# Kernel tuning notes

Measured on AMD Instinct MI355X. Metric: run time of the kernel, lower is better.

Reference implementation:

```python
import jax, jax.numpy as jnp
import numpy as np

NHEAD = 8  # from init_kwargs
EPS = 1e-5  # nn.LayerNorm default


def _ln(x, w, b):
    mu = jnp.mean(x, axis=-1, keepdims=True)
    var = jnp.mean(jnp.square(x - mu), axis=-1, keepdims=True)
    return (x - mu) * jax.lax.rsqrt(var + EPS) * w + b


def setup_inputs() -> dict:
    key = jax.random.key(0)
    L, D, FF, B, S = 4, 256, 512, 2, 4096
    ks = jax.random.split(key, 14)
    s = 0.02
    inp = {
        "seq": jax.random.normal(ks[0], (B, S, D), jnp.float32),
        "Wqkv": jax.random.normal(ks[1], (L, 3 * D, D), jnp.float32) * s,
        "bqkv": jnp.zeros((L, 3 * D), jnp.float32),
        "Wo": jax.random.normal(ks[2], (L, D, D), jnp.float32) * s,
        "bo": jnp.zeros((L, D), jnp.float32),
        "ln1_w": jnp.ones((L, D), jnp.float32),
        "ln1_b": jnp.zeros((L, D), jnp.float32),
        "ln2_w": jnp.ones((L, D), jnp.float32),
        "ln2_b": jnp.zeros((L, D), jnp.float32),
        "W1": jax.random.normal(ks[3], (L, FF, D), jnp.float32) * s,
        "b1": jnp.zeros((L, FF), jnp.float32),
        "W2": jax.random.normal(ks[4], (L, D, FF), jnp.float32) * s,
        "b2": jnp.zeros((L, D), jnp.float32),
        "n_ctx": 2048,
    }
    return inp


def _forward(seq, Wqkv, bqkv, Wo, bo, ln1_w, ln1_b, ln2_w, ln2_b, W1, b1, W2, b2, n_ctx):
    B, S, D = seq.shape
    H = NHEAD
    hd = D // H
    scale = 1.0 / np.sqrt(hd).astype(np.float32)
    x = seq
    L = Wqkv.shape[0]
    for l in range(L):
        # pre-norm self-attention block (norm_first=True)
        h = _ln(x, ln1_w[l], ln1_b[l])
        qkv = h @ Wqkv[l].T + bqkv[l]            # [B,S,3D]
        q, k, v = jnp.split(qkv, 3, axis=-1)
        q = q.reshape(B, S, H, hd)
        # Mask structure: every token (context AND query) may only attend to
        # context keys [:n_ctx] -> keys/values restricted up-front, no dense
        # [S,S] score matrix and no explicit mask needed.
        kc = k[:, :n_ctx].reshape(B, n_ctx, H, hd)
        vc = v[:, :n_ctx].reshape(B, n_ctx, H, hd)
        scores = jnp.einsum('bqhd,bkhd->bhqk', q, kc) * scale  # [B,H,S,n_ctx]
        att = jax.nn.softmax(scores, axis=-1)
        o = jnp.einsum('bhqk,bkhd->bqhd', att, vc).reshape(B, S, D)
        x = x + o @ Wo[l].T + bo[l]
        # pre-norm feed-forward block, exact (erf) GELU as in PyTorch 'gelu'
        h2 = _ln(x, ln2_w[l], ln2_b[l])
        x = x + jax.nn.gelu(h2 @ W1[l].T + b1[l], approximate=False) @ W2[l].T + b2[l]
    return x


def reference(seq, Wqkv, bqkv, Wo, bo, ln1_w, ln1_b, ln2_w, ln2_b, W1, b1, W2, b2, n_ctx):
    return _forward(seq, Wqkv, bqkv, Wo, bo, ln1_w, ln1_b, ln2_w, ln2_b, W1, b1, W2, b2, n_ctx)
```

## Files before the change

### kernel.cpp

```cpp
#include <hip/hip_runtime.h>
#include <hip/hip_bf16.h>

#define BB 2
#define SS 4096
#define DD 256
#define FFD 512
#define NLAYER 4
#define NHEAD 8
#define HD 32
#define QKVD 768
#define NROWS 8192
#define NCTX 2048

typedef unsigned short u16;
typedef unsigned int   u32;
typedef __attribute__((ext_vector_type(8))) short short8;
typedef __attribute__((ext_vector_type(4))) short sv4;
typedef __attribute__((ext_vector_type(4))) float f32x4;

#if __has_builtin(__builtin_amdgcn_exp2f)
#define EXP2(x) __builtin_amdgcn_exp2f(x)
#else
#define EXP2(x) exp2f(x)
#endif

__device__ __forceinline__ float bf2f(u32 u) { return __uint_as_float(u << 16); }
__device__ __forceinline__ u16 f2bu(float f) {
    union { __hip_bfloat16 h; u16 u; } cv; cv.h = __float2bfloat16(f); return cv.u;
}
__device__ __forceinline__ float gelu_f(float v) {
    return 0.5f * v * (1.0f + erff(v * 0.70710678118654752f));
}

__global__ __launch_bounds__(256) void init_kernel(
        const float* __restrict__ s0, const float* __restrict__ s1,
        const float* __restrict__ s2, const float* __restrict__ s3,
        u16* __restrict__ d0, u16* __restrict__ d1,
        u16* __restrict__ d2, u16* __restrict__ d3,
        const float* __restrict__ seq, float* __restrict__ x,
        const float* __restrict__ lw, const float* __restrict__ lb,
        u16* __restrict__ hln) {
    int blk = blockIdx.x;
    if (blk < 2048) {
        const float* s; u16* d; int base;
        if (blk < 768)       { s = s0; d = d0; base = blk; }
        else if (blk < 1024) { s = s1; d = d1; base = blk - 768; }
        else if (blk < 1536) { s = s2; d = d2; base = blk - 1024; }
        else                 { s = s3; d = d3; base = blk - 1536; }
        int i = (base * 256 + threadIdx.x) * 4;
        float4 v = *reinterpret_cast<const float4*>(s + i);
        uint2 o;
        o.x = (u32)f2bu(v.x) | ((u32)f2bu(v.y) << 16);
        o.y = (u32)f2bu(v.z) | ((u32)f2bu(v.w) << 16);
        *reinterpret_cast<uint2*>(d + i) = o;
    } else {
        int row = (blk - 2048) * 4 + (threadIdx.x >> 6);
        int lane = threadIdx.x & 63;
        int c = lane * 4;
        float4 v = *reinterpret_cast<const float4*>(seq + (size_t)row * DD + c);
        *reinterpret_cast<float4*>(x + (size_t)row * DD + c) = v;
        float s  = v.x + v.y + v.z + v.w;
        float sq = v.x*v.x + v.y*v.y + v.z*v.z + v.w*v.w;
        #pragma unroll
        for (int off = 32; off >= 1; off >>= 1) {
            s  += __shfl_xor(s, off);
            sq += __shfl_xor(sq, off);
        }
        float mu   = s * (1.0f / DD);
        float var  = sq * (1.0f / DD) - mu * mu;
        float rstd = rsqrtf(var + 1e-5f);
        float4 wv = *reinterpret_cast<const float4*>(lw + c);
        float4 bv = *reinterpret_cast<const float4*>(lb + c);
        float o0 = (v.x - mu) * rstd * wv.x + bv.x;
        float o1 = (v.y - mu) * rstd * wv.y + bv.y;
        float o2 = (v.z - mu) * rstd * wv.z + bv.z;
        float o3 = (v.w - mu) * rstd * wv.w + bv.w;
        uint2 o;
        o.x = (u32)f2bu(o0) | ((u32)f2bu(o1) << 16);
        o.y = (u32)f2bu(o2) | ((u32)f2bu(o3) << 16);
        *reinterpret_cast<uint2*>(hln + (size_t)row * DD + c) = o;
    }
}

__global__ void ln_kernel(const float* __restrict__ x, const float* __restrict__ w,
                          const float* __restrict__ b, u16* __restrict__ out) {
    int row = blockIdx.x * 4 + (threadIdx.x >> 6);
    int lane = threadIdx.x & 63;
    int c = lane * 4;
    float4 v = *reinterpret_cast<const float4*>(x + (size_t)row * DD + c);
    float s  = v.x + v.y + v.z + v.w;
    float sq = v.x*v.x + v.y*v.y + v.z*v.z + v.w*v.w;
    #pragma unroll
    for (int off = 32; off >= 1; off >>= 1) {
        s  += __shfl_xor(s, off);
        sq += __shfl_xor(sq, off);
    }
    float mu   = s * (1.0f / DD);
    float var  = sq * (1.0f / DD) - mu * mu;
    float rstd = rsqrtf(var + 1e-5f);
    float4 wv = *reinterpret_cast<const float4*>(w + c);
    float4 bv = *reinterpret_cast<const float4*>(b + c);
    float o0 = (v.x - mu) * rstd * wv.x + bv.x;
    float o1 = (v.y - mu) * rstd * wv.y + bv.y;
    float o2 = (v.z - mu) * rstd * wv.z + bv.z;
    float o3 = (v.w - mu) * rstd * wv.w + bv.w;
    uint2 o;
    o.x = (u32)f2bu(o0) | ((u32)f2bu(o1) << 16);
    o.y = (u32)f2bu(o2) | ((u32)f2bu(o3) << 16);
    *reinterpret_cast<uint2*>(out + (size_t)row * DD + c) = o;
}

template<int TM, int ACT, int RES, int WV>
__global__ __launch_bounds__(256) void mfma_gemm(
        const u16* __restrict__ A, const u16* __restrict__ W, const float* __restrict__ bias,
        float* __restrict__ outf, u16* __restrict__ outb, u16* __restrict__ vtg,
        int N, int K) {
    constexpr int MI = TM / 32;
    __shared__ __align__(16) u16 As[TM][136];
    __shared__ __align__(16) u16 Ws[64][136];
    int tid = threadIdx.x;
    int wave = tid >> 6, lane = tid & 63, la = lane & 15, quad = lane >> 4;
    int wm = (wave & 1) * (TM / 2), wn = (wave >> 1) * 32;
    int m0 = blockIdx.y * TM, n0 = blockIdx.x * 64;
    f32x4 acc[MI][2];
    #pragma unroll
    for (int mi = 0; mi < MI; mi++)
        #pragma unroll
        for (int ni = 0; ni < 2; ni++)
            acc[mi][ni] = (f32x4){0.f, 0.f, 0.f, 0.f};

    int ar = tid >> 4, ac = (tid & 15) * 8;
    for (int k0 = 0; k0 < K; k0 += 128) {
        #pragma unroll
        for (int p = 0; p < TM / 16; p++)
            *reinterpret_cast<uint4*>(&As[ar + p*16][ac]) =
                *reinterpret_cast<const uint4*>(&A[(size_t)(m0 + ar + p*16) * K + k0 + ac]);
        #pragma unroll
        for (int p = 0; p < 4; p++)
            *reinterpret_cast<uint4*>(&Ws[ar + p*16][ac]) =
                *reinterpret_cast<const uint4*>(&W[(size_t)(n0 + ar + p*16) * K + k0 + ac]);
        __syncthreads();
        #pragma unroll
        for (int kh = 0; kh < 4; kh++) {
            short8 af[MI], bf[2];
            #pragma unroll
            for (int mi = 0; mi < MI; mi++)
                af[mi] = *reinterpret_cast<const short8*>(&As[wm + mi*16 + la][kh*32 + quad*8]);
            #pragma unroll
            for (int ni = 0; ni < 2; ni++)
                bf[ni] = *reinterpret_cast<const short8*>(&Ws[wn + ni*16 + la][kh*32 + quad*8]);
            #pragma unroll
            for (int mi = 0; mi < MI; mi++)
                #pragma unroll
                for (int ni = 0; ni < 2; ni++)
                    acc[mi][ni] = __builtin_amdgcn_mfma_f32_16x16x32_bf16(af[mi], bf[ni], acc[mi][ni], 0, 0, 0);
        }
        __syncthreads();
    }

    #pragma unroll
    for (int mi = 0; mi < MI; mi++) {
        #pragma unroll
        for (int ni = 0; ni < 2; ni++) {
            int n = n0 + wn + ni*16 + la;
            float bv = bias[n];
            #pragma unroll
            for (int r = 0; r < 4; r++) {
                int m = m0 + wm + mi*16 + quad*4 + r;
                float v = acc[mi][ni][r] + bv;
                if (ACT) v = gelu_f(v);
                if (RES) outf[(size_t)m * N + n] += v;
                else     outb[(size_t)m * N + n] = f2bu(v);
            }
        }
    }

    if (WV) {
        if ((n0 >= 2*DD) && ((m0 & (SS-1)) < NCTX)) {
            int b = m0 >> 12;
            int kb = ((m0 + wm) & (SS-1)) + quad*8;
            #pragma unroll
            for (int mi = 0; mi < MI; mi++) {
                int chunk = kb + (mi >> 1)*32 + (mi & 1)*4;
                #pragma unroll
                for (int ni = 0; ni < 2; ni++) {
                    int n = n0 + wn + ni*16 + la;
                    int vc = n - 2*DD;
                    float bv = bias[n];
                    u16* dst = &vtg[((size_t)((b << 3) + (vc >> 5)) * 32 + (vc & 31)) * NCTX + chunk];
                    uint2 w;
                    w.x = (u32)f2bu(acc[mi][ni][0] + bv) | ((u32)f2bu(acc[mi][ni][1] + bv) << 16);
                    w.y = (u32)f2bu(acc[mi][ni][2] + bv) | ((u32)f2bu(acc[mi][ni][3] + bv) << 16);
                    *reinterpret_cast<uint2*>(dst) = w;
                }
            }
        }
    }
}

#define SCL2 0.2550437f
#define SH2  11.5415603f
__global__ __launch_bounds__(512, 4) void mfma_attn(const u16* __restrict__ qkv,
                                                    const u16* __restrict__ vtg,
                                                    u16* __restrict__ out) {
    __shared__ __align__(16) u16 smem[9728];
    u16 (*Ks)[64][40] = reinterpret_cast<u16(*)[64][40]>(smem);
    u16 (*Vt)[32][72] = reinterpret_cast<u16(*)[32][72]>(smem + 5120);

    int tid = threadIdx.x;
    int wv = tid >> 6, lane = tid & 63, la = lane & 15, quad = lane >> 4;
    int qw = wv & 3, ksp = wv >> 2;
    int bh = blockIdx.y, qidx = blockIdx.x;
    int b = bh >> 3, hh = bh & 7;
    size_t tokbase = (size_t)b * SS;
    int qb = qidx * 128 + qw * 32;

    short8 qf[2];
    #pragma unroll
    for (int qt = 0; qt < 2; qt++) {
        uint4 u = *reinterpret_cast<const uint4*>(
            &qkv[(tokbase + qb + qt*16 + la) * QKVD + hh*32 + quad*8]);
        union { short8 v; u16 e[8]; } qa;
        u32 w[4] = {u.x, u.y, u.z, u.w};
        #pragma unroll
        for (int i = 0; i < 4; i++) {
            qa.e[2*i]   = f2bu(bf2f(w[i] & 0xffffu) * SCL2);
            qa.e[2*i+1] = f2bu(bf2f(w[i] >> 16) * SCL2);
        }
        qf[qt] = qa.v;
    }

    f32x4 o[2][2];
    #pragma unroll
    for (int i = 0; i < 2; i++)
        #pragma unroll
        for (int j = 0; j < 2; j++) o[i][j] = (f32x4){0.f, 0.f, 0.f, 0.f};
    f32x4 l_acc[2];
    l_acc[0] = (f32x4){0.f, 0.f, 0.f, 0.f};
    l_acc[1] = (f32x4){0.f, 0.f, 0.f, 0.f};
    const f32x4 cinit = (f32x4){-SH2, -SH2, -SH2, -SH2};
    short8 onesf;
    { union { short8 v; u16 e[8]; } t;
      #pragma unroll
      for (int i = 0; i < 8; i++) t.e[i] = 0x3F80;
      onesf = t.v; }

    int sr = tid >> 2, sk = (tid & 3) * 8;
    int hs = sr >> 6, krow = sr & 63;
    int vr = tid >> 4, vc = (tid & 15) * 8;
    int vh = vc >> 6, vcol = vc & 63;
    const u16* kgp = &qkv[(tokbase + hs*1024 + krow) * QKVD + DD + hh*32 + sk];
    const u16* vgp = &vtg[((size_t)bh*32 + vr) * NCTX + vh*1024 + vcol];
    uint4 kreg = *reinterpret_cast<const uint4*>(kgp);
    uint4 vreg = *reinterpret_cast<const uint4*>(vgp);

    for (int step = 0; step < 16; step++) {
        *reinterpret_cast<uint4*>(&Ks[hs][krow][sk]) = kreg;
        *reinterpret_cast<uint4*>(&Vt[vh][vr][vcol]) = vreg;
        __syncthreads();
        if (step < 15) {
            kreg = *reinterpret_cast<const uint4*>(kgp + (size_t)(step+1)*64*QKVD);
            vreg = *reinterpret_cast<const uint4*>(vgp + (step+1)*64);
        }

        #pragma unroll
        for (int c = 0; c < 2; c++) {
            short8 kf0 = *reinterpret_cast<const short8*>(&Ks[ksp][c*32 + la][quad*8]);
            short8 kf1 = *reinterpret_cast<const short8*>(&Ks[ksp][c*32 + 16 + la][quad*8]);
            f32x4 s00 = __builtin_amdgcn_mfma_f32_16x16x32_bf16(kf0, qf[0], cinit, 0, 0, 0);
            f32x4 s10 = __builtin_amdgcn_mfma_f32_16x16x32_bf16(kf1, qf[0], cinit, 0, 0, 0);
            f32x4 s01 = __builtin_amdgcn_mfma_f32_16x16x32_bf16(kf0, qf[1], cinit, 0, 0, 0);
            f32x4 s11 = __builtin_amdgcn_mfma_f32_16x16x32_bf16(kf1, qf[1], cinit, 0, 0, 0);

            union { uint4 u; short8 v; } pf0, pf1;
            {
                u32 a0 = __float_as_uint(EXP2(s00[0])), a1 = __float_as_uint(EXP2(s00[1]));
                u32 a2 = __float_as_uint(EXP2(s00[2])), a3 = __float_as_uint(EXP2(s00[3]));
                u32 b0 = __float_as_uint(EXP2(s10[0])), b1 = __float_as_uint(EXP2(s10[1]));
                u32 b2 = __float_as_uint(EXP2(s10[2])), b3 = __float_as_uint(EXP2(s10[3]));
                pf0.u.x = __builtin_amdgcn_perm(a1, a0, 0x07060302u);
                pf0.u.y = __builtin_amdgcn_perm(a3, a2, 0x07060302u);
                pf0.u.z = __builtin_amdgcn_perm(b1, b0, 0x07060302u);
                pf0.u.w = __builtin_amdgcn_perm(b3, b2, 0x07060302u);
            }
            {
                u32 a0 = __float_as_uint(EXP2(s01[0])), a1 = __float_as_uint(EXP2(s01[1]));
                u32 a2 = __float_as_uint(EXP2(s01[2])), a3 = __float_as_uint(EXP2(s01[3]));
                u32 b0 = __float_as_uint(EXP2(s11[0])), b1 = __float_as_uint(EXP2(s11[1]));
                u32 b2 = __float_as_uint(EXP2(s11[2])), b3 = __float_as_uint(EXP2(s11[3]));
                pf1.u.x = __builtin_amdgcn_perm(a1, a0, 0x07060302u);
                pf1.u.y = __builtin_amdgcn_perm(a3, a2, 0x07060302u);
                pf1.u.z = __builtin_amdgcn_perm(b1, b0, 0x07060302u);
                pf1.u.w = __builtin_amdgcn_perm(b3, b2, 0x07060302u);
            }

            l_acc[0] = __builtin_amdgcn_mfma_f32_16x16x32_bf16(onesf, pf0.v, l_acc[0], 0, 0, 0);
            l_acc[1] = __builtin_amdgcn_mfma_f32_16x16x32_bf16(onesf, pf1.v, l_acc[1], 0, 0, 0);

            short8 vf0 = *reinterpret_cast<const short8*>(&Vt[ksp][la][c*32 + quad*8]);
            short8 vf1 = *reinterpret_cast<const short8*>(&Vt[ksp][16 + la][c*32 + quad*8]);
            o[0][0] = __builtin_amdgcn_mfma_f32_16x16x32_bf16(vf0, pf0.v, o[0][0], 0, 0, 0);
            o[0][1] = __builtin_amdgcn_mfma_f32_16x16x32_bf16(vf0, pf1.v, o[0][1], 0, 0, 0);
            o[1][0] = __builtin_amdgcn_mfma_f32_16x16x32_bf16(vf1, pf0.v, o[1][0], 0, 0, 0);
            o[1][1] = __builtin_amdgcn_mfma_f32_16x16x32_bf16(vf1, pf1.v, o[1][1], 0, 0, 0);
        }
        __syncthreads();
    }

    float* obuf = reinterpret_cast<float*>(smem);
    if (wv >= 4) {
        int idx = (qw * 64 + lane) * 18;
        #pragma unroll
        for (int mio = 0; mio < 2; mio++)
            #pragma unroll
            for (int qt = 0; qt < 2; qt++)
                #pragma unroll
                for (int r = 0; r < 4; r++)
                    obuf[idx + mio*8 + qt*4 + r] = o[mio][qt][r];
        obuf[idx + 16] = l_acc[0][0];
        obuf[idx + 17] = l_acc[1][0];
    }
    __syncthreads();
    if (wv < 4) {
        int idx = (qw * 64 + lane) * 18;
        #pragma unroll
        for (int mio = 0; mio < 2; mio++)
            #pragma unroll
            for (int qt = 0; qt < 2; qt++)
                #pragma unroll
                for (int r = 0; r < 4; r++)
                    o[mio][qt][r] += obuf[idx + mio*8 + qt*4 + r];
        float liq[2];
        liq[0] = 1.0f / (l_acc[0][0] + obuf[idx + 16]);
        liq[1] = 1.0f / (l_acc[1][0] + obuf[idx + 17]);
        #pragma unroll
        for (int qt = 0; qt < 2; qt++) {
            float li = liq[qt];
            size_t token = tokbase + qb + qt*16 + la;
            #pragma unroll
            for (int mio = 0; mio < 2; mio++) {
                uint2 w;
                w.x = (u32)f2bu(o[mio][qt][0] * li) | ((u32)f2bu(o[mio][qt][1] * li) << 16);
                w.y = (u32)f2bu(o[mio][qt][2] * li) | ((u32)f2bu(o[mio][qt][3] * li) << 16);
                *reinterpret_cast<uint2*>(&out[token * DD + hh*32 + mio*16 + quad*4]) = w;
            }
        }
    }
}

extern "C" void kernel_launch(void* const* d_in, const int* in_sizes, int n_in,
                              void* d_out, int out_size, void* d_ws, size_t ws_size,
                              hipStream_t stream) {
    const float* seq   = (const float*)d_in[0];
    const float* Wqkv  = (const float*)d_in[1];
    const float* bqkv  = (const float*)d_in[2];
    const float* Wo    = (const float*)d_in[3];
    const float* bo    = (const float*)d_in[4];
    const float* ln1w  = (const float*)d_in[5];
    const float* ln1b  = (const float*)d_in[6];
    const float* ln2w  = (const float*)d_in[7];
    const float* ln2b  = (const float*)d_in[8];
    const float* W1    = (const float*)d_in[9];
    const float* b1    = (const float*)d_in[10];
    const float* W2    = (const float*)d_in[11];
    const float* b2    = (const float*)d_in[12];

    float* x    = (float*)d_out;
    char* wsb   = (char*)d_ws;
    u16*  qkv   = (u16*)wsb;
    u16*  ff    = qkv;
    u16*  h     = (u16*)(wsb + 12582912);
    u16*  hln   = (u16*)(wsb + 16777216);
    u16*  wbf   = (u16*)(wsb + 20971520);
    u16*  vtg   = (u16*)(wsb + 25165824);
    u16* wqkv_b = wbf;
    u16* wo_b   = wbf + 786432;
    u16* w1_b   = wbf + 1048576;
    u16* w2_b   = wbf + 1572864;

    init_kernel<<<4096, 256, 0, stream>>>(Wqkv, Wo, W1, W2, wqkv_b, wo_b, w1_b, w2_b,
                                          seq, x, ln1w, ln1b, hln);

    for (int l = 0; l < NLAYER; l++) {
        mfma_gemm<128,0,0,1><<<dim3(QKVD/64, NROWS/128), 256, 0, stream>>>(
            hln, wqkv_b + (size_t)l*QKVD*DD, bqkv + l*QKVD, nullptr, qkv, vtg, QKVD, DD);
        mfma_attn<<<dim3(SS/128, BB*NHEAD), 512, 0, stream>>>(qkv, vtg, h);
        mfma_gemm<64,0,1,0><<<dim3(DD/64, NROWS/64), 256, 0, stream>>>(
            h, wo_b + (size_t)l*DD*DD, bo + l*DD, x, nullptr, nullptr, DD, DD);
        ln_kernel<<<NROWS/4, 256, 0, stream>>>(x, ln2w + l*DD, ln2b + l*DD, hln);
        mfma_gemm<128,1,0,0><<<dim3(FFD/64, NROWS/128), 256, 0, stream>>>(
            hln, w1_b + (size_t)l*FFD*DD, b1 + l*FFD, nullptr, ff, nullptr, FFD, DD);
        mfma_gemm<64,0,1,0><<<dim3(DD/64, NROWS/64), 256, 0, stream>>>(
            ff, w2_b + (size_t)l*DD*FFD, b2 + l*DD, x, nullptr, nullptr, DD, FFD);
        if (l < NLAYER - 1)
            ln_kernel<<<NROWS/4, 256, 0, stream>>>(x, ln1w + (l+1)*DD, ln1b + (l+1)*DD, hln);
    }
}
```

Measured before the change: 390.3 us.

## Fuse LayerNorm into GEMM prologue via partial row stats; widen attention KV tiles

Removes the standalone LayerNorm kernels. The residual GEMMs (Wo, W2) now write per-row partial sums and sums of squares for each 32-column slice. The QKV and FF1 GEMMs read fp32 x directly, reduce those partials into mean and rstd, and normalize while staging A into shared memory. A per-XCD block swizzle is added to the LN-fused GEMMs, and the attention kernel now loads 128 keys per step instead of 64, with double the LDS. The trade-off is that each N-block recomputes the normalization and reads fp32 activations instead of bf16, in exchange for fewer launches and no round trip of the normalized tensor.

Result: slower. 407.6 us (+4.4%).

```diff
diff --git a/kernel.cpp b/kernel.cpp
--- a/kernel.cpp
+++ b/kernel.cpp
@@ -15,7 +15,6 @@
 typedef unsigned short u16;
 typedef unsigned int   u32;
 typedef __attribute__((ext_vector_type(8))) short short8;
-typedef __attribute__((ext_vector_type(4))) short sv4;
 typedef __attribute__((ext_vector_type(4))) float f32x4;
 
 #if __has_builtin(__builtin_amdgcn_exp2f)
@@ -38,8 +37,7 @@
         u16* __restrict__ d0, u16* __restrict__ d1,
         u16* __restrict__ d2, u16* __restrict__ d3,
         const float* __restrict__ seq, float* __restrict__ x,
-        const float* __restrict__ lw, const float* __restrict__ lb,
-        u16* __restrict__ hln) {
+        float* __restrict__ part) {
     int blk = blockIdx.x;
     if (blk < 2048) {
         const float* s; u16* d; int base;
@@ -59,69 +57,63 @@
         int c = lane * 4;
         float4 v = *reinterpret_cast<const float4*>(seq + (size_t)row * DD + c);
         *reinterpret_cast<float4*>(x + (size_t)row * DD + c) = v;
-        float s  = v.x + v.y + v.z + v.w;
-        float sq = v.x*v.x + v.y*v.y + v.z*v.z + v.w*v.w;
-        #pragma unroll
-        for (int off = 32; off >= 1; off >>= 1) {
-            s  += __shfl_xor(s, off);
-            sq += __shfl_xor(sq, off);
-        }
-        float mu   = s * (1.0f / DD);
-        float var  = sq * (1.0f / DD) - mu * mu;
-        float rstd = rsqrtf(var + 1e-5f);
-        float4 wv = *reinterpret_cast<const float4*>(lw + c);
-        float4 bv = *reinterpret_cast<const float4*>(lb + c);
-        float o0 = (v.x - mu) * rstd * wv.x + bv.x;
-        float o1 = (v.y - mu) * rstd * wv.y + bv.y;
-        float o2 = (v.z - mu) * rstd * wv.z + bv.z;
-        float o3 = (v.w - mu) * rstd * wv.w + bv.w;
-        uint2 o;
-        o.x = (u32)f2bu(o0) | ((u32)f2bu(o1) << 16);
-        o.y = (u32)f2bu(o2) | ((u32)f2bu(o3) << 16);
-        *reinterpret_cast<uint2*>(hln + (size_t)row * DD + c) = o;
-    }
-}
-
-__global__ void ln_kernel(const float* __restrict__ x, const float* __restrict__ w,
-                          const float* __restrict__ b, u16* __restrict__ out) {
-    int row = blockIdx.x * 4 + (threadIdx.x >> 6);
-    int lane = threadIdx.x & 63;
-    int c = lane * 4;
-    float4 v = *reinterpret_cast<const float4*>(x + (size_t)row * DD + c);
-    float s  = v.x + v.y + v.z + v.w;
-    float sq = v.x*v.x + v.y*v.y + v.z*v.z + v.w*v.w;
-    #pragma unroll
-    for (int off = 32; off >= 1; off >>= 1) {
-        s  += __shfl_xor(s, off);
-        sq += __shfl_xor(sq, off);
-    }
-    float mu   = s * (1.0f / DD);
-    float var  = sq * (1.0f / DD) - mu * mu;
-    float rstd = rsqrtf(var + 1e-5f);
-    float4 wv = *reinterpret_cast<const float4*>(w + c);
-    float4 bv = *reinterpret_cast<const float4*>(b + c);
-    float o0 = (v.x - mu) * rstd * wv.x + bv.x;
-    float o1 = (v.y - mu) * rstd * wv.y + bv.y;
-    float o2 = (v.z - mu) * rstd * wv.z + bv.z;
-    float o3 = (v.w - mu) * rstd * wv.w + bv.w;
-    uint2 o;
-    o.x = (u32)f2bu(o0) | ((u32)f2bu(o1) << 16);
-    o.y = (u32)f2bu(o2) | ((u32)f2bu(o3) << 16);
-    *reinterpret_cast<uint2*>(out + (size_t)row * DD + c) = o;
-}
-
-template<int TM, int ACT, int RES, int WV>
+        float s4  = v.x + v.y + v.z + v.w;
+        float sq4 = v.x*v.x + v.y*v.y + v.z*v.z + v.w*v.w;
+        #pragma unroll
+        for (int off = 1; off <= 4; off <<= 1) {
+            s4  += __shfl_xor(s4, off);
+            sq4 += __shfl_xor(sq4, off);
+        }
+        if ((lane & 7) == 0)
+            reinterpret_cast<float2*>(part)[(lane >> 3) * NROWS + row] =
+                make_float2(s4, sq4);
+    }
+}
+
+template<int TM, int ACT, int RES, int WV, int ALN, int WP>
 __global__ __launch_bounds__(256) void mfma_gemm(
-        const u16* __restrict__ A, const u16* __restrict__ W, const float* __restrict__ bias,
-        float* __restrict__ outf, u16* __restrict__ outb, u16* __restrict__ vtg,
-        int N, int K) {
+        const u16* __restrict__ A, const float* __restrict__ Af,
+        const float* __restrict__ part, const float* __restrict__ lnw,
+        const float* __restrict__ lnb,
+        const u16* __restrict__ W, const float* __restrict__ bias,
+        float* __restrict__ outf, u16* __restrict__ outb,
+        u16* __restrict__ vtg, float* __restrict__ partw, int N, int K) {
     constexpr int MI = TM / 32;
     __shared__ __align__(16) u16 As[TM][136];
     __shared__ __align__(16) u16 Ws[64][136];
+    __shared__ float rowstat[ALN ? TM : 1][2];
     int tid = threadIdx.x;
     int wave = tid >> 6, lane = tid & 63, la = lane & 15, quad = lane >> 4;
     int wm = (wave & 1) * (TM / 2), wn = (wave >> 1) * 32;
-    int m0 = blockIdx.y * TM, n0 = blockIdx.x * 64;
+    int bx = blockIdx.x, by = blockIdx.y;
+    if (ALN) {
+        int nx = gridDim.x, ny = gridDim.y;
+        int flat = by * nx + bx;
+        int xcd = flat & 7, j = flat >> 3;
+        int perx = ny >> 3;
+        by = xcd * perx + j / nx;
+        bx = j % nx;
+    }
+    int m0 = by * TM, n0 = bx * 64;
+
+    if (ALN) {
+        for (int t = tid; t < TM; t += 256) {
+            int row = m0 + t;
+            float S = 0.f, Q = 0.f;
+            #pragma unroll
+            for (int s = 0; s < 8; s++) {
+                float2 p = reinterpret_cast<const float2*>(part)[s * NROWS + row];
+                S += p.x; Q += p.y;
+            }
+            float mu  = S * (1.0f / DD);
+            float var = Q * (1.0f / DD) - mu * mu;
+            float rstd = rsqrtf(var + 1e-5f);
+            rowstat[t][0] = rstd;
+            rowstat[t][1] = mu;
+        }
+        __syncthreads();
+    }
+
     f32x4 acc[MI][2];
     #pragma unroll
     for (int mi = 0; mi < MI; mi++)
@@ -131,10 +123,36 @@
 
     int ar = tid >> 4, ac = (tid & 15) * 8;
     for (int k0 = 0; k0 < K; k0 += 128) {
-        #pragma unroll
-        for (int p = 0; p < TM / 16; p++)
-            *reinterpret_cast<uint4*>(&As[ar + p*16][ac]) =
-                *reinterpret_cast<const uint4*>(&A[(size_t)(m0 + ar + p*16) * K + k0 + ac]);
+        if (ALN) {
+            float lw[8], lb[8];
+            *reinterpret_cast<float4*>(&lw[0]) = *reinterpret_cast<const float4*>(&lnw[k0 + ac]);
+            *reinterpret_cast<float4*>(&lw[4]) = *reinterpret_cast<const float4*>(&lnw[k0 + ac + 4]);
+            *reinterpret_cast<float4*>(&lb[0]) = *reinterpret_cast<const float4*>(&lnb[k0 + ac]);
+            *reinterpret_cast<float4*>(&lb[4]) = *reinterpret_cast<const float4*>(&lnb[k0 + ac + 4]);
+            #pragma unroll
+            for (int p = 0; p < TM / 16; p++) {
+                int row = ar + p * 16;
+                float rstd = rowstat[row][0], mu = rowstat[row][1];
+                float4 v0 = *reinterpret_cast<const float4*>(&Af[(size_t)(m0 + row) * K + k0 + ac]);
+                float4 v1 = *reinterpret_cast<const float4*>(&Af[(size_t)(m0 + row) * K + k0 + ac + 4]);
+                float e[8] = {v0.x, v0.y, v0.z, v0.w, v1.x, v1.y, v1.z, v1.w};
+                u16 hh[8];
+                #pragma unroll
+                for (int j = 0; j < 8; j++)
+                    hh[j] = f2bu((e[j] - mu) * rstd * lw[j] + lb[j]);
+                uint4 pk;
+                pk.x = (u32)hh[0] | ((u32)hh[1] << 16);
+                pk.y = (u32)hh[2] | ((u32)hh[3] << 16);
+                pk.z = (u32)hh[4] | ((u32)hh[5] << 16);
+                pk.w = (u32)hh[6] | ((u32)hh[7] << 16);
+                *reinterpret_cast<uint4*>(&As[row][ac]) = pk;
+            }
+        } else {
+            #pragma unroll
+            for (int p = 0; p < TM / 16; p++)
+                *reinterpret_cast<uint4*>(&As[ar + p*16][ac]) =
+                    *reinterpret_cast<const uint4*>(&A[(size_t)(m0 + ar + p*16) * K + k0 + ac]);
+        }
         #pragma unroll
         for (int p = 0; p < 4; p++)
             *reinterpret_cast<uint4*>(&Ws[ar + p*16][ac]) =
@@ -158,19 +176,65 @@
         __syncthreads();
     }
 
-    #pragma unroll
-    for (int mi = 0; mi < MI; mi++) {
-        #pragma unroll
-        for (int ni = 0; ni < 2; ni++) {
-            int n = n0 + wn + ni*16 + la;
-            float bv = bias[n];
-            #pragma unroll
-            for (int r = 0; r < 4; r++) {
-                int m = m0 + wm + mi*16 + quad*4 + r;
-                float v = acc[mi][ni][r] + bv;
-                if (ACT) v = gelu_f(v);
-                if (RES) outf[(size_t)m * N + n] += v;
-                else     outb[(size_t)m * N + n] = f2bu(v);
+    if (RES) {
+        float t[MI][2][4];
+        #pragma unroll
+        for (int mi = 0; mi < MI; mi++) {
+            #pragma unroll
+            for (int ni = 0; ni < 2; ni++) {
+                int n = n0 + wn + ni*16 + la;
+                float bv = bias[n];
+                #pragma unroll
+                for (int r = 0; r < 4; r++) {
+                    int m = m0 + wm + mi*16 + quad*4 + r;
+                    float xo = outf[(size_t)m * N + n];
+                    float tv = xo + acc[mi][ni][r] + bv;
+                    outf[(size_t)m * N + n] = tv;
+                    t[mi][ni][r] = tv;
+                }
+            }
+        }
+        if (WP) {
+            int slice = (n0 + wn) >> 5;
+            #pragma unroll
+            for (int mi = 0; mi < MI; mi++) {
+                float s[4], q[4];
+                #pragma unroll
+                for (int r = 0; r < 4; r++) {
+                    s[r] = t[mi][0][r] + t[mi][1][r];
+                    q[r] = t[mi][0][r]*t[mi][0][r] + t[mi][1][r]*t[mi][1][r];
+                }
+                #pragma unroll
+                for (int off = 1; off <= 8; off <<= 1)
+                    #pragma unroll
+                    for (int r = 0; r < 4; r++) {
+                        s[r] += __shfl_xor(s[r], off);
+                        q[r] += __shfl_xor(q[r], off);
+                    }
+                if (la == 0) {
+                    #pragma unroll
+                    for (int r = 0; r < 4; r++) {
+                        int row = m0 + wm + mi*16 + quad*4 + r;
+                        reinterpret_cast<float2*>(partw)[slice * NROWS + row] =
+                            make_float2(s[r], q[r]);
+                    }
+                }
+            }
+        }
+    } else {
+        #pragma unroll
+        for (int mi = 0; mi < MI; mi++) {
+            #pragma unroll
+            for (int ni = 0; ni < 2; ni++) {
+                int n = n0 + wn + ni*16 + la;
+                float bv = bias[n];
+                #pragma unroll
+                for (int r = 0; r < 4; r++) {
+                    int m = m0 + wm + mi*16 + quad*4 + r;
+                    float v = acc[mi][ni][r] + bv;
+                    if (ACT) v = gelu_f(v);
+                    outb[(size_t)m * N + n] = f2bu(v);
+                }
             }
         }
     }
@@ -203,9 +267,9 @@
 __global__ __launch_bounds__(512, 4) void mfma_attn(const u16* __restrict__ qkv,
                                                     const u16* __restrict__ vtg,
                                                     u16* __restrict__ out) {
-    __shared__ __align__(16) u16 smem[9728];
-    u16 (*Ks)[64][40] = reinterpret_cast<u16(*)[64][40]>(smem);
-    u16 (*Vt)[32][72] = reinterpret_cast<u16(*)[32][72]>(smem + 5120);
+    __shared__ __align__(16) u16 smem[18944];
+    u16 (*Ks)[128][40] = reinterpret_cast<u16(*)[128][40]>(smem);
+    u16 (*Vt)[32][136] = reinterpret_cast<u16(*)[32][136]>(smem + 10240);
 
     int tid = threadIdx.x;
     int wv = tid >> 6, lane = tid & 63, la = lane & 15, quad = lane >> 4;
@@ -246,25 +310,30 @@
       onesf = t.v; }
 
     int sr = tid >> 2, sk = (tid & 3) * 8;
-    int hs = sr >> 6, krow = sr & 63;
     int vr = tid >> 4, vc = (tid & 15) * 8;
-    int vh = vc >> 6, vcol = vc & 63;
-    const u16* kgp = &qkv[(tokbase + hs*1024 + krow) * QKVD + DD + hh*32 + sk];
-    const u16* vgp = &vtg[((size_t)bh*32 + vr) * NCTX + vh*1024 + vcol];
-    uint4 kreg = *reinterpret_cast<const uint4*>(kgp);
-    uint4 vreg = *reinterpret_cast<const uint4*>(vgp);
-
-    for (int step = 0; step < 16; step++) {
-        *reinterpret_cast<uint4*>(&Ks[hs][krow][sk]) = kreg;
-        *reinterpret_cast<uint4*>(&Vt[vh][vr][vcol]) = vreg;
+    const u16* kgp0 = &qkv[(tokbase + sr) * QKVD + DD + hh*32 + sk];
+    const u16* kgp1 = &qkv[(tokbase + 1024 + sr) * QKVD + DD + hh*32 + sk];
+    const u16* vgp  = &vtg[((size_t)bh*32 + vr) * NCTX + vc];
+    uint4 kreg0 = *reinterpret_cast<const uint4*>(kgp0);
+    uint4 kreg1 = *reinterpret_cast<const uint4*>(kgp1);
+    uint4 vreg0 = *reinterpret_cast<const uint4*>(vgp);
+    uint4 vreg1 = *reinterpret_cast<const uint4*>(vgp + 1024);
+
+    for (int step = 0; step < 8; step++) {
+        *reinterpret_cast<uint4*>(&Ks[0][sr][sk]) = kreg0;
+        *reinterpret_cast<uint4*>(&Ks[1][sr][sk]) = kreg1;
+        *reinterpret_cast<uint4*>(&Vt[0][vr][vc]) = vreg0;
+        *reinterpret_cast<uint4*>(&Vt[1][vr][vc]) = vreg1;
         __syncthreads();
-        if (step < 15) {
-            kreg = *reinterpret_cast<const uint4*>(kgp + (size_t)(step+1)*64*QKVD);
-            vreg = *reinterpret_cast<const uint4*>(vgp + (step+1)*64);
-        }
-
-        #pragma unroll
-        for (int c = 0; c < 2; c++) {
+        if (step < 7) {
+            kreg0 = *reinterpret_cast<const uint4*>(kgp0 + (size_t)(step+1)*128*QKVD);
+            kreg1 = *reinterpret_cast<const uint4*>(kgp1 + (size_t)(step+1)*128*QKVD);
+            vreg0 = *reinterpret_cast<const uint4*>(vgp + (step+1)*128);
+            vreg1 = *reinterpret_cast<const uint4*>(vgp + 1024 + (step+1)*128);
+        }
+
+        #pragma unroll
+        for (int c = 0; c < 4; c++) {
             short8 kf0 = *reinterpret_cast<const short8*>(&Ks[ksp][c*32 + la][quad*8]);
             short8 kf1 = *reinterpret_cast<const short8*>(&Ks[ksp][c*32 + 16 + la][quad*8]);
             f32x4 s00 = __builtin_amdgcn_mfma_f32_16x16x32_bf16(kf0, qf[0], cinit, 0, 0, 0);
@@ -370,7 +439,7 @@
     u16*  qkv   = (u16*)wsb;
     u16*  ff    = qkv;
     u16*  h     = (u16*)(wsb + 12582912);
-    u16*  hln   = (u16*)(wsb + 16777216);
+    float* part = (float*)(wsb + 16777216);
     u16*  wbf   = (u16*)(wsb + 20971520);
     u16*  vtg   = (u16*)(wsb + 25165824);
     u16* wqkv_b = wbf;
@@ -379,20 +448,25 @@
     u16* w2_b   = wbf + 1572864;
 
     init_kernel<<<4096, 256, 0, stream>>>(Wqkv, Wo, W1, W2, wqkv_b, wo_b, w1_b, w2_b,
-                                          seq, x, ln1w, ln1b, hln);
+                                          seq, x, part);
 
     for (int l = 0; l < NLAYER; l++) {
-        mfma_gemm<128,0,0,1><<<dim3(QKVD/64, NROWS/128), 256, 0, stream>>>(
-            hln, wqkv_b + (size_t)l*QKVD*DD, bqkv + l*QKVD, nullptr, qkv, vtg, QKVD, DD);
+        mfma_gemm<128,0,0,1,1,0><<<dim3(QKVD/64, NROWS/128), 256, 0, stream>>>(
+            nullptr, x, part, ln1w + l*DD, ln1b + l*DD,
+            wqkv_b + (size_t)l*QKVD*DD, bqkv + l*QKVD,
+            nullptr, qkv, vtg, nullptr, QKVD, DD);
         mfma_attn<<<dim3(SS/128, BB*NHEAD), 512, 0, stream>>>(qkv, vtg, h);
-        mfma_gemm<64,0,1,0><<<dim3(DD/64, NROWS/64), 256, 0, stream>>>(
-            h, wo_b + (size_t)l*DD*DD, bo + l*DD, x, nullptr, nullptr, DD, DD);
-        ln_kernel<<<NROWS/4, 256, 0, stream>>>(x, ln2w + l*DD, ln2b + l*DD, hln);
-        mfma_gemm<128,1,0,0><<<dim3(FFD/64, NROWS/128), 256, 0, stream>>>(
-            hln, w1_b + (size_t)l*FFD*DD, b1 + l*FFD, nullptr, ff, nullptr, FFD, DD);
-        mfma_gemm<64,0,1,0><<<dim3(DD/64, NROWS/64), 256, 0, stream>>>(
-            ff, w2_b + (size_t)l*DD*FFD, b2 + l*DD, x, nullptr, nullptr, DD, FFD);
-        if (l < NLAYER - 1)
-            ln_kernel<<<NROWS/4, 256, 0, stream>>>(x, ln1w + (l+1)*DD, ln1b + (l+1)*DD, hln);
-    }
-}
+        mfma_gemm<64,0,1,0,0,1><<<dim3(DD/64, NROWS/64), 256, 0, stream>>>(
+            h, nullptr, nullptr, nullptr, nullptr,
+            wo_b + (size_t)l*DD*DD, bo + l*DD,
+            x, nullptr, nullptr, part, DD, DD);
+        mfma_gemm<128,1,0,0,1,0><<<dim3(FFD/64, NROWS/128), 256, 0, stream>>>(
+            nullptr, x, part, ln2w + l*DD, ln2b + l*DD,
+            w1_b + (size_t)l*FFD*DD, b1 + l*FFD,
+            nullptr, ff, nullptr, nullptr, FFD, DD);
+        mfma_gemm<64,0,1,0,0,1><<<dim3(DD/64, NROWS/64), 256, 0, stream>>>(
+            ff, nullptr, nullptr, nullptr, nullptr,
+            w2_b + (size_t)l*DD*FFD, b2 + l*DD,
+            x, nullptr, nullptr, part, DD, FFD);
+    }
+}
```
